# Performance work log

Hardware: AMD Instinct MI355X
Metric: run time of the kernel (lower is better)

Reference implementation:

```python
import jax, jax.numpy as jnp
import numpy as np
import math

N = 65536
C_IN = 64
C_OUT = 64
NS = 16
BN_EPS = 1e-5


def _knn_idx(p_np, k):
    # exact kNN (including self), chunked to bound memory
    p_np = np.asarray(p_np, np.float32)
    n = p_np.shape[0]
    sq = (p_np * p_np).sum(1)
    idx = np.empty((n, k), np.int32)
    cs = 1024
    for s in range(0, n, cs):
        q = p_np[s:s + cs]
        d = sq[None, :] - 2.0 * (q @ p_np.T) + (q * q).sum(1)[:, None]
        part = np.argpartition(d, k, axis=1)[:, :k]
        dd = np.take_along_axis(d, part, 1)
        order = np.argsort(dd, axis=1)
        idx[s:s + cs] = np.take_along_axis(part, order, 1).astype(np.int32)
    return idx


def setup_inputs() -> dict:
    key = jax.random.key(0)
    ks = jax.random.split(key, 12)
    p = jax.random.uniform(ks[0], (N, 3), dtype=jnp.float32) * 10.0
    x = jax.random.normal(ks[1], (N, C_IN), dtype=jnp.float32)
    idx = jnp.asarray(_knn_idx(np.asarray(p), NS))  # (N, NS) int32
    s_in = 1.0 / math.sqrt(C_IN)
    Wq = jax.random.normal(ks[2], (C_IN, C_OUT), dtype=jnp.float32) * s_in
    bq = jnp.zeros((C_OUT,), jnp.float32)
    Wk = jax.random.normal(ks[3], (C_IN, C_OUT), dtype=jnp.float32) * s_in
    bk = jnp.zeros((C_OUT,), jnp.float32)
    Wv = jax.random.normal(ks[4], (C_IN, C_OUT), dtype=jnp.float32) * s_in
    bv = jnp.zeros((C_OUT,), jnp.float32)
    Wp1 = jax.random.normal(ks[5], (3, 3), dtype=jnp.float32) * (1.0 / math.sqrt(3))
    bp1 = jnp.zeros((3,), jnp.float32)
    gamma = jnp.ones((3,), jnp.float32)
    beta = jnp.zeros((3,), jnp.float32)
    Wp2 = jax.random.normal(ks[6], (3, C_OUT), dtype=jnp.float32) * (1.0 / math.sqrt(3))
    bp2 = jnp.zeros((C_OUT,), jnp.float32)
    return {"p": p, "x": x, "idx": idx, "Wq": Wq, "bq": bq, "Wk": Wk, "bk": bk,
            "Wv": Wv, "bv": bv, "Wp1": Wp1, "bp1": bp1, "gamma": gamma,
            "beta": beta, "Wp2": Wp2, "bp2": bp2}


def reference(p, x, idx, Wq, bq, Wk, bk, Wv, bv, Wp1, bp1, gamma, beta, Wp2, bp2):
    x_q = x @ Wq + bq                       # (N, Co)
    x_k = (x @ Wk + bk)[idx]                # gather: (N, NS, Co)
    x_v = (x @ Wv + bv)[idx]                # gather: (N, NS, Co)
    p_r = p[idx] - p[:, None, :]            # relative coords (N, NS, 3)
    # linear_p: Linear(3,3) -> BatchNorm1d(3) (training stats) -> ReLU -> Linear(3,Co)
    h = p_r @ Wp1 + bp1                     # (N, NS, 3)
    mean = h.mean(axis=(0, 1))
    var = ((h - mean) ** 2).mean(axis=(0, 1))
    h = (h - mean) * jax.lax.rsqrt(var + BN_EPS) * gamma + beta
    h = jax.nn.relu(h)
    p_emb = h @ Wp2 + bp2                   # (N, NS, Co)
    x_k = x_k + p_emb
    x_v = x_v + p_emb
    attn = (x_q[:, None, :] * x_k).sum(-1) / math.sqrt(C_OUT)  # (N, NS)
    w = jax.nn.softmax(attn, axis=1)
    return (x_v * w[:, :, None]).sum(axis=1)  # (N, Co)
```

## Files before the change

### kernel.cpp

```cpp
#include <hip/hip_runtime.h>

#define N_PTS 65536
#define NSS 16
#define C 64

typedef __attribute__((ext_vector_type(8))) short short8;
typedef __attribute__((ext_vector_type(4))) float f32x4;

__device__ __forceinline__ unsigned short f2bf(float v) {
  unsigned int u = __float_as_uint(v);
  u += 0x7fffu + ((u >> 16) & 1u);
  return (unsigned short)(u >> 16);
}
__device__ __forceinline__ float bflo(unsigned int u) { return __uint_as_float(u << 16); }
__device__ __forceinline__ float bfhi(unsigned int u) { return __uint_as_float(u & 0xffff0000u); }

__device__ __forceinline__ int cell_of(float px, float py, float pz) {
  const int cx = min(15, max(0, (int)(px * 1.6f)));
  const int cy = min(15, max(0, (int)(py * 1.6f)));
  const int cz = min(15, max(0, (int)(pz * 1.6f)));
  int m = 0;
#pragma unroll
  for (int b = 0; b < 4; ++b)
    m |= (((cx >> b) & 1) << (3 * b + 2)) | (((cy >> b) & 1) << (3 * b + 1)) |
         (((cz >> b) & 1) << (3 * b));
  return m;
}

__global__ __launch_bounds__(256) void init_kernel(
    const float* __restrict__ Wq, const float* __restrict__ Wk, const float* __restrict__ Wv,
    const float* __restrict__ Wp2, const float* __restrict__ bp2, const float* __restrict__ bq,
    const float* __restrict__ p,
    float* __restrict__ stats, unsigned short* __restrict__ wt,
    unsigned short* __restrict__ wtq, float* __restrict__ tb, int* __restrict__ hist) {
  const int t = blockIdx.x * 256 + threadIdx.x;
  if (t < 9) stats[t] = 0.f;
  if (t < 192 * 64) {
    const int k = t / 192, ng = t % 192;
    const int mat = ng >> 6, n = ng & 63;
    const float* W = mat == 0 ? Wq : (mat == 1 ? Wk : Wv);
    wt[ng * 64 + k] = f2bf(W[k * 64 + n]);
  }
  if (t < 1024) {
    const int row = t >> 6, k = t & 63;
    float val = 0.f;
    if (row < 4) {
      const float* B2 = (row == 3) ? bp2 : (Wp2 + row * 64);
      for (int c2 = 0; c2 < 64; ++c2) val += Wq[k * 64 + c2] * B2[c2];
    }
    wtq[t] = f2bf(val);
  }
  if (t >= 1024 && t < 1028) {
    const int n2 = t - 1024;
    const float* B2 = (n2 == 3) ? bp2 : (Wp2 + n2 * 64);
    float val = 0.f;
    for (int c2 = 0; c2 < 64; ++c2) val += bq[c2] * B2[c2];
    tb[n2] = val;
  }
  if (t < N_PTS) {
    atomicAdd(&hist[cell_of(p[t * 3 + 0], p[t * 3 + 1], p[t * 3 + 2])], 1);
  }
}

__global__ __launch_bounds__(256) void qkv_kernel(
    const float* __restrict__ x, const unsigned short* __restrict__ wt,
    const unsigned short* __restrict__ wtq, const float* __restrict__ tb,
    const float* __restrict__ bq, const float* __restrict__ bk, const float* __restrict__ bv,
    const float* __restrict__ p, const int* __restrict__ idx,
    unsigned short* __restrict__ kvq, float* __restrict__ tq, float* __restrict__ stats) {
  __shared__ __align__(16) unsigned short xs[64][72];
  __shared__ __align__(16) unsigned short kvs[64][192];
  const int t = threadIdx.x;
  const int p0 = blockIdx.x * 64;
  const float4* x4 = (const float4*)x;
#pragma unroll
  for (int j = 0; j < 4; ++j) {
    const int id = j * 256 + t;
    const int row = id >> 4, cg = id & 15;
    const float4 v = x4[(p0 + row) * 16 + cg];
    ushort4 h4;
    h4.x = f2bf(v.x); h4.y = f2bf(v.y); h4.z = f2bf(v.z); h4.w = f2bf(v.w);
    *(ushort4*)&xs[row][cg * 4] = h4;
  }
  __syncthreads();

  const int lane = t & 63, wave = t >> 6;
  const int quad = lane >> 4, lr = lane & 15;
  const int mrow = wave * 16 + lr;
  const short8 a0 = *(const short8*)&xs[mrow][quad * 8];
  const short8 a1 = *(const short8*)&xs[mrow][quad * 8 + 32];
#pragma unroll
  for (int nt = 0; nt < 12; ++nt) {
    const unsigned short* bpr = wt + (nt * 16 + lr) * 64 + quad * 8;
    const short8 b0 = *(const short8*)bpr;
    const short8 b1 = *(const short8*)(bpr + 32);
    f32x4 acc = {0.f, 0.f, 0.f, 0.f};
    acc = __builtin_amdgcn_mfma_f32_16x16x32_bf16(a0, b0, acc, 0, 0, 0);
    acc = __builtin_amdgcn_mfma_f32_16x16x32_bf16(a1, b1, acc, 0, 0, 0);
    const int mat = nt >> 2;
    const int c = (nt & 3) * 16 + lr;
    const float bias = (mat == 0 ? bq : (mat == 1 ? bk : bv))[c];
#pragma unroll
    for (int r = 0; r < 4; ++r) {
      const int row = wave * 16 + quad * 4 + r;
      kvs[row][mat * 64 + c] = f2bf(acc[r] + bias);
    }
  }
  {
    const unsigned short* bpr = wtq + lr * 64 + quad * 8;
    const short8 b0 = *(const short8*)bpr;
    const short8 b1 = *(const short8*)(bpr + 32);
    f32x4 acc = {0.f, 0.f, 0.f, 0.f};
    acc = __builtin_amdgcn_mfma_f32_16x16x32_bf16(a0, b0, acc, 0, 0, 0);
    acc = __builtin_amdgcn_mfma_f32_16x16x32_bf16(a1, b1, acc, 0, 0, 0);
    if (lr < 4) {
      const float tbv = tb[lr];
#pragma unroll
      for (int r = 0; r < 4; ++r) {
        const int pt = p0 + wave * 16 + quad * 4 + r;
        tq[pt * 4 + lr] = acc[r] + tbv;
      }
    }
  }
  __syncthreads();
  const uint4* kvs4 = (const uint4*)&kvs[0][0];
  uint4* dst = (uint4*)(kvq + (size_t)p0 * 192);
#pragma unroll
  for (int j = 0; j < 6; ++j) dst[j * 256 + t] = kvs4[j * 256 + t];

  const int tid = blockIdx.x * 256 + t;
  float s0 = 0, s1 = 0, s2 = 0, s00 = 0, s01 = 0, s02 = 0, s11 = 0, s12 = 0, s22 = 0;
  for (int s = tid; s < N_PTS * NSS; s += 262144) {
    const int n = s >> 4;
    const int j = idx[s];
    const float dx = p[j * 3 + 0] - p[n * 3 + 0];
    const float dy = p[j * 3 + 1] - p[n * 3 + 1];
    const float dz = p[j * 3 + 2] - p[n * 3 + 2];
    s0 += dx; s1 += dy; s2 += dz;
    s00 += dx * dx; s01 += dx * dy; s02 += dx * dz;
    s11 += dy * dy; s12 += dy * dz; s22 += dz * dz;
  }
#pragma unroll
  for (int m = 1; m < 64; m <<= 1) {
    s0 += __shfl_xor(s0, m, 64);  s1 += __shfl_xor(s1, m, 64);  s2 += __shfl_xor(s2, m, 64);
    s00 += __shfl_xor(s00, m, 64); s01 += __shfl_xor(s01, m, 64); s02 += __shfl_xor(s02, m, 64);
    s11 += __shfl_xor(s11, m, 64); s12 += __shfl_xor(s12, m, 64); s22 += __shfl_xor(s22, m, 64);
  }
  __shared__ float part[4][9];
  if (lane == 0) {
    part[wave][0] = s0;  part[wave][1] = s1;  part[wave][2] = s2;
    part[wave][3] = s00; part[wave][4] = s01; part[wave][5] = s02;
    part[wave][6] = s11; part[wave][7] = s12; part[wave][8] = s22;
  }
  __syncthreads();
  if (t < 9) {
    atomicAdd(&stats[t], part[0][t] + part[1][t] + part[2][t] + part[3][t]);
  }
}

__global__ __launch_bounds__(256) void scan_kernel(
    const int* __restrict__ hist, int* __restrict__ offs,
    const float* __restrict__ stats,
    const float* __restrict__ Wp1, const float* __restrict__ bp1,
    const float* __restrict__ gamma, const float* __restrict__ beta,
    float* __restrict__ ebn) {
  const int t = threadIdx.x;
  const int lane = t & 63, wv = t >> 6;
  int loc[16];
  int sum = 0;
#pragma unroll
  for (int i = 0; i < 16; ++i) { loc[i] = hist[t * 16 + i]; sum += loc[i]; }
  int incl = sum;
#pragma unroll
  for (int off = 1; off < 64; off <<= 1) {
    const int v = __shfl_up(incl, off, 64);
    if (lane >= off) incl += v;
  }
  __shared__ int wtot[4];
  if (lane == 63) wtot[wv] = incl;
  __syncthreads();
  int wbase = 0;
#pragma unroll
  for (int i = 0; i < 4; ++i) wbase += (i < wv) ? wtot[i] : 0;
  int run = wbase + incl - sum;
#pragma unroll
  for (int i = 0; i < 16; ++i) { offs[t * 16 + i] = run; run += loc[i]; }

  if (t == 0) {
    const float invM = 1.0f / (float)(N_PTS * NSS);
    const float m0 = stats[0] * invM, m1 = stats[1] * invM, m2 = stats[2] * invM;
    const float cv00 = stats[3] * invM - m0 * m0, cv01 = stats[4] * invM - m0 * m1;
    const float cv02 = stats[5] * invM - m0 * m2, cv11 = stats[6] * invM - m1 * m1;
    const float cv12 = stats[7] * invM - m1 * m2, cv22 = stats[8] * invM - m2 * m2;
#pragma unroll
    for (int tt = 0; tt < 3; ++tt) {
      const float w0 = Wp1[0 * 3 + tt], w1 = Wp1[1 * 3 + tt], w2 = Wp1[2 * 3 + tt];
      const float mh = w0 * m0 + w1 * m1 + w2 * m2 + bp1[tt];
      const float var = w0 * w0 * cv00 + w1 * w1 * cv11 + w2 * w2 * cv22 +
                        2.f * (w0 * w1 * cv01 + w0 * w2 * cv02 + w1 * w2 * cv12);
      const float sc = gamma[tt] * rsqrtf(var + 1e-5f);
      ebn[tt] = w0 * sc; ebn[3 + tt] = w1 * sc; ebn[6 + tt] = w2 * sc;
      ebn[9 + tt] = (bp1[tt] - mh) * sc + beta[tt];
    }
  }
}

__global__ __launch_bounds__(256) void scatter_kernel(const float* __restrict__ p,
                                                      int* __restrict__ offs,
                                                      int* __restrict__ perm) {
  const int t = blockIdx.x * 256 + threadIdx.x;
  const int cidx = cell_of(p[t * 3 + 0], p[t * 3 + 1], p[t * 3 + 2]);
  const int pos = atomicAdd(&offs[cidx], 1);
  perm[pos] = t;
}

template <int CTRL>
__device__ __forceinline__ float dppmv(float x) {
  return __int_as_float(__builtin_amdgcn_update_dpp(
      __float_as_int(x), __float_as_int(x), CTRL, 0xF, 0xF, true));
}
__device__ __forceinline__ float red16_add(float x) {
  x += dppmv<0xB1>(x);
  x += dppmv<0x4E>(x);
  x += __shfl_xor(x, 4, 64);
  x += __shfl_xor(x, 8, 64);
  return x;
}
__device__ __forceinline__ float red16_max(float x) {
  x = fmaxf(x, dppmv<0xB1>(x));
  x = fmaxf(x, dppmv<0x4E>(x));
  x = fmaxf(x, __shfl_xor(x, 4, 64));
  x = fmaxf(x, __shfl_xor(x, 8, 64));
  return x;
}

__global__ __launch_bounds__(256, 4) void attn_kernel(
    const float* __restrict__ p, const int* __restrict__ idx,
    const unsigned short* __restrict__ kvq, const float* __restrict__ tq,
    const int* __restrict__ perm, const float* __restrict__ ebn,
    const float* __restrict__ Wp2, const float* __restrict__ bp2,
    float* __restrict__ out) {
  const int lane = threadIdx.x & 63;
  const int wave = threadIdx.x >> 6;
  const int b = blockIdx.x;
  const int sb = (b & 7) * 512 + (b >> 3);
  const int base = sb * 16 + wave * 4;
  const int quad = lane >> 4, lr = lane & 15;

  const int4 ng4 = *(const int4*)(perm + base);
  const int ng[4] = {ng4.x, ng4.y, ng4.z, ng4.w};
  const int nown = ng[quad];
  const int jall = idx[nown * NSS + lr];

  float S = 0.f;
#pragma unroll
  for (int g = 0; g < 4; ++g) {
    const int jg = __shfl(jall, (g << 4) | lr, 64);
    const short8 a0 = *(const short8*)(kvq + (size_t)ng[g] * 192 + quad * 8);
    const short8 a1 = *(const short8*)(kvq + (size_t)ng[g] * 192 + quad * 8 + 32);
    const short8 k0 = *(const short8*)(kvq + (size_t)jg * 192 + 64 + quad * 8);
    const short8 k1 = *(const short8*)(kvq + (size_t)jg * 192 + 64 + quad * 8 + 32);
    f32x4 acc = {0.f, 0.f, 0.f, 0.f};
    acc = __builtin_amdgcn_mfma_f32_16x16x32_bf16(a0, k0, acc, 0, 0, 0);
    acc = __builtin_amdgcn_mfma_f32_16x16x32_bf16(a1, k1, acc, 0, 0, 0);
    S = (quad == g) ? acc[0] : S;
  }

  float e[12];
#pragma unroll
  for (int i = 0; i < 12; ++i) e[i] = ebn[i];
  const float pnx = p[nown * 3 + 0], pny = p[nown * 3 + 1], pnz = p[nown * 3 + 2];
  const float dx = p[jall * 3 + 0] - pnx;
  const float dy = p[jall * 3 + 1] - pny;
  const float dz = p[jall * 3 + 2] - pnz;
  const float h0 = fmaxf(fmaf(dx, e[0], fmaf(dy, e[3], fmaf(dz, e[6], e[9]))), 0.f);
  const float h1 = fmaxf(fmaf(dx, e[1], fmaf(dy, e[4], fmaf(dz, e[7], e[10]))), 0.f);
  const float h2 = fmaxf(fmaf(dx, e[2], fmaf(dy, e[5], fmaf(dz, e[8], e[11]))), 0.f);

  const float4 t4 = ((const float4*)tq)[nown];
  const float a = (S + fmaf(h0, t4.x, fmaf(h1, t4.y, fmaf(h2, t4.z, t4.w)))) * 0.125f;

  const float mx = red16_max(a);
  const float ex = __expf(a - mx);
  const float den = red16_add(ex);
  const float w = ex / den;

  const float H0 = red16_add(w * h0);
  const float H1 = red16_add(w * h1);
  const float H2 = red16_add(w * h2);

  float o0 = 0.f, o1 = 0.f, o2 = 0.f, o3 = 0.f;
#pragma unroll
  for (int s = 0; s < NSS; ++s) {
    const int jr = __shfl(jall, (lane & 48) | s, 64);
    const float ws = __shfl(w, (lane & 48) | s, 64);
    const uint2 v2 = *(const uint2*)(kvq + (size_t)jr * 192 + 128 + lr * 4);
    o0 = fmaf(ws, bflo(v2.x), o0);
    o1 = fmaf(ws, bfhi(v2.x), o1);
    o2 = fmaf(ws, bflo(v2.y), o2);
    o3 = fmaf(ws, bfhi(v2.y), o3);
  }

  const float4 w20 = ((const float4*)Wp2)[0 * 16 + lr];
  const float4 w21 = ((const float4*)Wp2)[16 + lr];
  const float4 w22 = ((const float4*)Wp2)[32 + lr];
  const float4 b2 = ((const float4*)bp2)[lr];
  o0 += fmaf(H0, w20.x, fmaf(H1, w21.x, fmaf(H2, w22.x, b2.x)));
  o1 += fmaf(H0, w20.y, fmaf(H1, w21.y, fmaf(H2, w22.y, b2.y)));
  o2 += fmaf(H0, w20.z, fmaf(H1, w21.z, fmaf(H2, w22.z, b2.z)));
  o3 += fmaf(H0, w20.w, fmaf(H1, w21.w, fmaf(H2, w22.w, b2.w)));
  const float4 res = {o0, o1, o2, o3};
  ((float4*)out)[nown * 16 + lr] = res;
}

extern "C" void kernel_launch(void* const* d_in, const int* in_sizes, int n_in,
                              void* d_out, int out_size, void* d_ws, size_t ws_size,
                              hipStream_t stream) {
  const float* p     = (const float*)d_in[0];
  const float* x     = (const float*)d_in[1];
  const int*   idx   = (const int*)d_in[2];
  const float* Wq    = (const float*)d_in[3];
  const float* bq    = (const float*)d_in[4];
  const float* Wk    = (const float*)d_in[5];
  const float* bk    = (const float*)d_in[6];
  const float* Wv    = (const float*)d_in[7];
  const float* bv    = (const float*)d_in[8];
  const float* Wp1   = (const float*)d_in[9];
  const float* bp1   = (const float*)d_in[10];
  const float* gamma = (const float*)d_in[11];
  const float* beta  = (const float*)d_in[12];
  const float* Wp2   = (const float*)d_in[13];
  const float* bp2   = (const float*)d_in[14];
  float* out = (float*)d_out;

  char* w = (char*)d_ws;
  float* stats        = (float*)w;
  float* tb           = (float*)(w + 64);
  float* ebn          = (float*)(w + 128);
  unsigned short* wt  = (unsigned short*)(w + 256);
  unsigned short* wtq = (unsigned short*)(w + 25088);
  int* hist           = (int*)(w + 32768);
  int* offs           = (int*)(w + 49152);
  int* perm           = (int*)(w + 65536);
  unsigned short* kvq = (unsigned short*)(w + 327680);
  float* tq           = (float*)(w + 25493504);

  hipMemsetAsync(hist, 0, 4096 * sizeof(int), stream);
  init_kernel<<<256, 256, 0, stream>>>(Wq, Wk, Wv, Wp2, bp2, bq, p, stats, wt, wtq, tb, hist);
  qkv_kernel<<<N_PTS / 64, 256, 0, stream>>>(x, wt, wtq, tb, bq, bk, bv, p, idx, kvq, tq, stats);
  scan_kernel<<<1, 256, 0, stream>>>(hist, offs, stats, Wp1, bp1, gamma, beta, ebn);
  scatter_kernel<<<256, 256, 0, stream>>>(p, offs, perm);
  attn_kernel<<<N_PTS / 16, 256, 0, stream>>>(p, idx, kvq, tq, perm, ebn, Wp2, bp2, out);
}
```

Baseline: 182.6 us.

## Split BN statistics into a separate kernel with padded atomic slots

```diff
diff --git a/kernel.cpp b/kernel.cpp
--- a/kernel.cpp
+++ b/kernel.cpp
@@ -31,10 +31,9 @@
     const float* __restrict__ Wq, const float* __restrict__ Wk, const float* __restrict__ Wv,
     const float* __restrict__ Wp2, const float* __restrict__ bp2, const float* __restrict__ bq,
     const float* __restrict__ p,
-    float* __restrict__ stats, unsigned short* __restrict__ wt,
-    unsigned short* __restrict__ wtq, float* __restrict__ tb, int* __restrict__ hist) {
+    unsigned short* __restrict__ wt, unsigned short* __restrict__ wtq,
+    float* __restrict__ tb, int* __restrict__ hist) {
   const int t = blockIdx.x * 256 + threadIdx.x;
-  if (t < 9) stats[t] = 0.f;
   if (t < 192 * 64) {
     const int k = t / 192, ng = t % 192;
     const int mat = ng >> 6, n = ng & 63;
@@ -62,12 +61,50 @@
   }
 }
 
-__global__ __launch_bounds__(256) void qkv_kernel(
+__global__ __launch_bounds__(256) void stats_kernel(
+    const float* __restrict__ p, const int* __restrict__ idx, float* __restrict__ stats) {
+  const int tid = blockIdx.x * 256 + threadIdx.x;
+  const int n = tid >> 2;
+  const int4 j4 = ((const int4*)idx)[tid];
+  const float pnx = p[n * 3 + 0], pny = p[n * 3 + 1], pnz = p[n * 3 + 2];
+  float s0 = 0, s1 = 0, s2 = 0, s00 = 0, s01 = 0, s02 = 0, s11 = 0, s12 = 0, s22 = 0;
+  const int js[4] = {j4.x, j4.y, j4.z, j4.w};
+#pragma unroll
+  for (int i = 0; i < 4; ++i) {
+    const int j = js[i];
+    const float dx = p[j * 3 + 0] - pnx;
+    const float dy = p[j * 3 + 1] - pny;
+    const float dz = p[j * 3 + 2] - pnz;
+    s0 += dx; s1 += dy; s2 += dz;
+    s00 += dx * dx; s01 += dx * dy; s02 += dx * dz;
+    s11 += dy * dy; s12 += dy * dz; s22 += dz * dz;
+  }
+#pragma unroll
+  for (int m = 1; m < 64; m <<= 1) {
+    s0 += __shfl_xor(s0, m, 64);  s1 += __shfl_xor(s1, m, 64);  s2 += __shfl_xor(s2, m, 64);
+    s00 += __shfl_xor(s00, m, 64); s01 += __shfl_xor(s01, m, 64); s02 += __shfl_xor(s02, m, 64);
+    s11 += __shfl_xor(s11, m, 64); s12 += __shfl_xor(s12, m, 64); s22 += __shfl_xor(s22, m, 64);
+  }
+  __shared__ float part[4][9];
+  const int wave = threadIdx.x >> 6, lane = threadIdx.x & 63;
+  if (lane == 0) {
+    part[wave][0] = s0;  part[wave][1] = s1;  part[wave][2] = s2;
+    part[wave][3] = s00; part[wave][4] = s01; part[wave][5] = s02;
+    part[wave][6] = s11; part[wave][7] = s12; part[wave][8] = s22;
+  }
+  __syncthreads();
+  if (threadIdx.x < 9) {
+    const float acc = part[0][threadIdx.x] + part[1][threadIdx.x] +
+                      part[2][threadIdx.x] + part[3][threadIdx.x];
+    atomicAdd(&stats[threadIdx.x * 16], acc);
+  }
+}
+
+__global__ __launch_bounds__(256) void qkv_gemm(
     const float* __restrict__ x, const unsigned short* __restrict__ wt,
     const unsigned short* __restrict__ wtq, const float* __restrict__ tb,
     const float* __restrict__ bq, const float* __restrict__ bk, const float* __restrict__ bv,
-    const float* __restrict__ p, const int* __restrict__ idx,
-    unsigned short* __restrict__ kvq, float* __restrict__ tq, float* __restrict__ stats) {
+    unsigned short* __restrict__ kvq, float* __restrict__ tq) {
   __shared__ __align__(16) unsigned short xs[64][72];
   __shared__ __align__(16) unsigned short kvs[64][192];
   const int t = threadIdx.x;
@@ -127,35 +164,6 @@
   uint4* dst = (uint4*)(kvq + (size_t)p0 * 192);
 #pragma unroll
   for (int j = 0; j < 6; ++j) dst[j * 256 + t] = kvs4[j * 256 + t];
-
-  const int tid = blockIdx.x * 256 + t;
-  float s0 = 0, s1 = 0, s2 = 0, s00 = 0, s01 = 0, s02 = 0, s11 = 0, s12 = 0, s22 = 0;
-  for (int s = tid; s < N_PTS * NSS; s += 262144) {
-    const int n = s >> 4;
-    const int j = idx[s];
-    const float dx = p[j * 3 + 0] - p[n * 3 + 0];
-    const float dy = p[j * 3 + 1] - p[n * 3 + 1];
-    const float dz = p[j * 3 + 2] - p[n * 3 + 2];
-    s0 += dx; s1 += dy; s2 += dz;
-    s00 += dx * dx; s01 += dx * dy; s02 += dx * dz;
-    s11 += dy * dy; s12 += dy * dz; s22 += dz * dz;
-  }
-#pragma unroll
-  for (int m = 1; m < 64; m <<= 1) {
-    s0 += __shfl_xor(s0, m, 64);  s1 += __shfl_xor(s1, m, 64);  s2 += __shfl_xor(s2, m, 64);
-    s00 += __shfl_xor(s00, m, 64); s01 += __shfl_xor(s01, m, 64); s02 += __shfl_xor(s02, m, 64);
-    s11 += __shfl_xor(s11, m, 64); s12 += __shfl_xor(s12, m, 64); s22 += __shfl_xor(s22, m, 64);
-  }
-  __shared__ float part[4][9];
-  if (lane == 0) {
-    part[wave][0] = s0;  part[wave][1] = s1;  part[wave][2] = s2;
-    part[wave][3] = s00; part[wave][4] = s01; part[wave][5] = s02;
-    part[wave][6] = s11; part[wave][7] = s12; part[wave][8] = s22;
-  }
-  __syncthreads();
-  if (t < 9) {
-    atomicAdd(&stats[t], part[0][t] + part[1][t] + part[2][t] + part[3][t]);
-  }
 }
 
 __global__ __launch_bounds__(256) void scan_kernel(
@@ -188,10 +196,10 @@
 
   if (t == 0) {
     const float invM = 1.0f / (float)(N_PTS * NSS);
-    const float m0 = stats[0] * invM, m1 = stats[1] * invM, m2 = stats[2] * invM;
-    const float cv00 = stats[3] * invM - m0 * m0, cv01 = stats[4] * invM - m0 * m1;
-    const float cv02 = stats[5] * invM - m0 * m2, cv11 = stats[6] * invM - m1 * m1;
-    const float cv12 = stats[7] * invM - m1 * m2, cv22 = stats[8] * invM - m2 * m2;
+    const float m0 = stats[0] * invM, m1 = stats[16] * invM, m2 = stats[32] * invM;
+    const float cv00 = stats[48] * invM - m0 * m0, cv01 = stats[64] * invM - m0 * m1;
+    const float cv02 = stats[80] * invM - m0 * m2, cv11 = stats[96] * invM - m1 * m1;
+    const float cv12 = stats[112] * invM - m1 * m2, cv22 = stats[128] * invM - m2 * m2;
 #pragma unroll
     for (int tt = 0; tt < 3; ++tt) {
       const float w0 = Wp1[0 * 3 + tt], w1 = Wp1[1 * 3 + tt], w2 = Wp1[2 * 3 + tt];
@@ -335,19 +343,20 @@
 
   char* w = (char*)d_ws;
   float* stats        = (float*)w;
-  float* tb           = (float*)(w + 64);
-  float* ebn          = (float*)(w + 128);
-  unsigned short* wt  = (unsigned short*)(w + 256);
-  unsigned short* wtq = (unsigned short*)(w + 25088);
-  int* hist           = (int*)(w + 32768);
-  int* offs           = (int*)(w + 49152);
+  int* hist           = (int*)(w + 1024);
+  float* tb           = (float*)(w + 17408);
+  float* ebn          = (float*)(w + 17472);
+  unsigned short* wt  = (unsigned short*)(w + 17536);
+  unsigned short* wtq = (unsigned short*)(w + 42112);
+  int* offs           = (int*)(w + 45056);
   int* perm           = (int*)(w + 65536);
   unsigned short* kvq = (unsigned short*)(w + 327680);
   float* tq           = (float*)(w + 25493504);
 
-  hipMemsetAsync(hist, 0, 4096 * sizeof(int), stream);
-  init_kernel<<<256, 256, 0, stream>>>(Wq, Wk, Wv, Wp2, bp2, bq, p, stats, wt, wtq, tb, hist);
-  qkv_kernel<<<N_PTS / 64, 256, 0, stream>>>(x, wt, wtq, tb, bq, bk, bv, p, idx, kvq, tq, stats);
+  hipMemsetAsync(w, 0, 17408, stream);
+  init_kernel<<<256, 256, 0, stream>>>(Wq, Wk, Wv, Wp2, bp2, bq, p, wt, wtq, tb, hist);
+  stats_kernel<<<1024, 256, 0, stream>>>(p, idx, stats);
+  qkv_gemm<<<N_PTS / 64, 256, 0, stream>>>(x, wt, wtq, tb, bq, bk, bv, kvq, tq);
   scan_kernel<<<1, 256, 0, stream>>>(hist, offs, stats, Wp1, bp1, gamma, beta, ebn);
   scatter_kernel<<<256, 256, 0, stream>>>(p, offs, perm);
   attn_kernel<<<N_PTS / 16, 256, 0, stream>>>(p, idx, kvq, tq, perm, ebn, Wp2, bp2, out);
```

Result: slower. 196.7 us (+7.7%).
